# Performance work log

Hardware: AMD Instinct MI355X
Metric: run time of the kernel (lower is better)

Reference implementation:

```python
import jax, jax.numpy as jnp
import numpy as np

N = 100000   # nodes
E = 800000   # edges
D = 128      # input dim
H = 128      # hidden dim
C = 2        # output classes
BN_EPS = 1e-5


def setup_inputs() -> dict:
    key = jax.random.key(0)
    ks = jax.random.split(key, 24)
    glorot = lambda k, shape: jax.random.normal(k, shape, dtype=jnp.float32) * np.sqrt(2.0 / (shape[0] + shape[1]))
    inp = {
        "x": jax.random.normal(ks[0], (N, D), dtype=jnp.float32),
        "edge_index": jax.random.randint(ks[1], (2, E), 0, N, dtype=jnp.int64),
        "W0": glorot(ks[2], (D, H)), "b0": jnp.zeros((H,), jnp.float32),
        "W1": glorot(ks[3], (H, H)), "b1": jnp.zeros((H,), jnp.float32),
        "W2": glorot(ks[4], (H, H)), "b2": jnp.zeros((H,), jnp.float32),
        "W3": glorot(ks[5], (H, C)), "b3": jnp.zeros((C,), jnp.float32),
        # BatchNorm (eval mode: running stats)
        "bn0_g": jax.random.normal(ks[6], (H,), dtype=jnp.float32) * 0.1 + 1.0,
        "bn0_b": jax.random.normal(ks[7], (H,), dtype=jnp.float32) * 0.1,
        "bn0_m": jax.random.normal(ks[8], (H,), dtype=jnp.float32) * 0.1,
        "bn0_v": jax.random.uniform(ks[9], (H,), dtype=jnp.float32) + 0.5,
        "bn1_g": jax.random.normal(ks[10], (H,), dtype=jnp.float32) * 0.1 + 1.0,
        "bn1_b": jax.random.normal(ks[11], (H,), dtype=jnp.float32) * 0.1,
        "bn1_m": jax.random.normal(ks[12], (H,), dtype=jnp.float32) * 0.1,
        "bn1_v": jax.random.uniform(ks[13], (H,), dtype=jnp.float32) + 0.5,
    }
    return inp


def _gcn_conv(h, W, b, src, dst, norm, self_norm):
    # GCNConv: D^-1/2 (A + I) D^-1/2 (h W) + b
    hw = h @ W                                             # [N, out]
    msg = hw[src] * norm[:, None]                          # [E, out] gather
    agg = jax.ops.segment_sum(msg, dst, num_segments=N)    # [N, out] scatter-add
    return agg + hw * self_norm[:, None] + b


def _bn_eval(h, g, b, m, v):
    return (h - m) * (g * jax.lax.rsqrt(v + BN_EPS)) + b


def reference(x, edge_index, W0, b0, W1, b1, W2, b2, W3, b3,
              bn0_g, bn0_b, bn0_m, bn0_v, bn1_g, bn1_b, bn1_m, bn1_v):
    src, dst = edge_index[0], edge_index[1]
    # symmetric normalization with self-loops
    deg = jax.ops.segment_sum(jnp.ones((E,), jnp.float32), dst, num_segments=N) + 1.0
    dis = jax.lax.rsqrt(deg)                 # deg >= 1, no inf
    norm = dis[src] * dis[dst]               # per-edge norm
    self_norm = dis * dis                    # self-loop norm

    # layer 0 (eval mode: dropout is identity)
    h = jax.nn.relu(_gcn_conv(x, W0, b0, src, dst, norm, self_norm))
    # layer 1: conv -> bn -> relu -> residual
    h_prev = h
    h = _gcn_conv(h, W1, b1, src, dst, norm, self_norm)
    h = jax.nn.relu(_bn_eval(h, bn0_g, bn0_b, bn0_m, bn0_v)) + h_prev
    # layer 2
    h_prev = h
    h = _gcn_conv(h, W2, b2, src, dst, norm, self_norm)
    h = jax.nn.relu(_bn_eval(h, bn1_g, bn1_b, bn1_m, bn1_v)) + h_prev
    # output layer
    h = _gcn_conv(h, W3, b3, src, dst, norm, self_norm)
    return jax.nn.log_softmax(h, axis=1)
```

## Files before the change

kernel.cpp:

```cpp
#include <hip/hip_runtime.h>
#include <hip/hip_bf16.h>
#include <type_traits>

#define NN 100000
#define NE 800000
#define HD 128
#define BN_EPS 1e-5f
#define NB_E_C 3125

typedef __bf16 bf16x8 __attribute__((ext_vector_type(8)));
typedef float  f32x4  __attribute__((ext_vector_type(4)));
typedef float  f32x2  __attribute__((ext_vector_type(2)));


__global__ __launch_bounds__(256) void count_prep_k(const int* __restrict__ ei, int* __restrict__ count,
                                                    int* __restrict__ rank,
                                                    const float* __restrict__ W0, const float* __restrict__ W1,
                                                    const float* __restrict__ W2, __bf16* __restrict__ WT,
                                                    const float* __restrict__ g0, const float* __restrict__ b0,
                                                    const float* __restrict__ m0, const float* __restrict__ v0,
                                                    const float* __restrict__ g1, const float* __restrict__ b1,
                                                    const float* __restrict__ m1, const float* __restrict__ v1,
                                                    float* __restrict__ A0, float* __restrict__ B0,
                                                    float* __restrict__ A1, float* __restrict__ B1) {
    int bid = blockIdx.x;
    int tid = threadIdx.x;
    if (bid < NB_E_C) {
        int e = bid * 256 + tid;
        if (e < NE) rank[e] = atomicAdd(&count[ei[NE + e]], 1);
    } else if (bid < NB_E_C + 3) {
        int w = bid - NB_E_C;
        const float* Ws[3] = {W0, W1, W2};
        const float* W = Ws[w];
        __bf16* T = WT + w * (HD * HD);
        #pragma unroll 4
        for (int it = 0; it < 64; ++it) {
            int idx = it * 256 + tid;
            int n = idx >> 7, k = idx & 127;
            T[idx] = (__bf16)W[k * HD + n];
        }
    } else {
        if (tid < 128) {
            float a = g0[tid] * rsqrtf(v0[tid] + BN_EPS);
            A0[tid] = a; B0[tid] = b0[tid] - m0[tid] * a;
        } else {
            int u = tid - 128;
            float a = g1[u] * rsqrtf(v1[u] + BN_EPS);
            A1[u] = a; B1[u] = b1[u] - m1[u] * a;
        }
    }
}

__global__ __launch_bounds__(256) void scan1_k(const int* __restrict__ count,
                                               int* __restrict__ rp, int* __restrict__ bsums,
                                               float* __restrict__ dis, float* __restrict__ selfn) {
    __shared__ int sm[256];
    int tid = threadIdx.x;
    int i = blockIdx.x * 256 + tid;
    int v = (i < NN) ? count[i] : 0;
    if (i < NN) {
        float deg = (float)v + 1.0f;
        float di = rsqrtf(deg);
        dis[i] = di;
        selfn[i] = di * di;
    }
    sm[tid] = v; __syncthreads();
    for (int off = 1; off < 256; off <<= 1) {
        int t = (tid >= off) ? sm[tid - off] : 0;
        __syncthreads();
        sm[tid] += t;
        __syncthreads();
    }
    if (i < NN) rp[i] = sm[tid] - v;
    if (tid == 255) bsums[blockIdx.x] = sm[tid];
}

__global__ __launch_bounds__(256) void scan23_k(int* __restrict__ rp, const int* __restrict__ bsums, int nb) {
    __shared__ int sm[256];
    int tid = threadIdx.x;
    int b = blockIdx.x;
    int partial = 0;
    for (int i = tid; i < b; i += 256) partial += bsums[i];
    sm[tid] = partial; __syncthreads();
    #pragma unroll
    for (int off = 128; off > 0; off >>= 1) {
        if (tid < off) sm[tid] += sm[tid + off];
        __syncthreads();
    }
    int prefix = sm[0];
    int i = b * 256 + tid;
    if (i < NN) rp[i] += prefix;
    if (i == 0) rp[NN] = NE;
}

__global__ __launch_bounds__(256) void scatter_k(const int* __restrict__ ei, const int* __restrict__ rp,
                                                 const int* __restrict__ rank, const float* __restrict__ dis,
                                                 uint2* __restrict__ edges) {
    int e = blockIdx.x * 256 + threadIdx.x;
    if (e >= NE) return;
    int s = ei[e], d = ei[NE + e];
    int pos = rp[d] + rank[e];
    edges[pos] = make_uint2((unsigned)s, __float_as_uint(dis[s] * dis[d]));
}


template <typename T>
__global__ __launch_bounds__(256, 5) void gemm128_k(const T* __restrict__ A, const __bf16* __restrict__ WTg,
                                                    __bf16* __restrict__ HW) {
    __shared__ __bf16 WL[128 * 128];
    const int tid = threadIdx.x;
    const int wid  = __builtin_amdgcn_readfirstlane(tid >> 6);
    const int lane = tid & 63;
    const int m = lane & 15, quad = lane >> 4;
    const int row_base = blockIdx.x * 64 + wid * 16;

    int r = row_base + m;
    if (r >= NN) r = NN - 1;
    bf16x8 afr[4];
    if constexpr (std::is_same<T, float>::value) {
        const float4* ap = (const float4*)(A + (size_t)r * HD);
        #pragma unroll
        for (int ks = 0; ks < 4; ++ks) {
            float4 x0 = ap[ks * 8 + quad * 2], x1 = ap[ks * 8 + quad * 2 + 1];
            bf16x8 a;
            a[0] = (__bf16)x0.x; a[1] = (__bf16)x0.y; a[2] = (__bf16)x0.z; a[3] = (__bf16)x0.w;
            a[4] = (__bf16)x1.x; a[5] = (__bf16)x1.y; a[6] = (__bf16)x1.z; a[7] = (__bf16)x1.w;
            afr[ks] = a;
        }
    } else {
        const bf16x8* ap = (const bf16x8*)(A + (size_t)r * HD);
        #pragma unroll
        for (int ks = 0; ks < 4; ++ks) afr[ks] = ap[ks * 4 + quad];
    }

    #pragma unroll
    for (int it = 0; it < 8; ++it) {
        int id = it * 256 + tid;
        int n = id >> 4, c = id & 15;
        int cs = c ^ (n >> 3);
        *(uint4*)&WL[n * 128 + cs * 8] = *(const uint4*)(WTg + n * HD + c * 8);
    }
    __syncthreads();

    f32x4 acc[8];
    #pragma unroll
    for (int ct = 0; ct < 8; ++ct) acc[ct] = (f32x4){0.f, 0.f, 0.f, 0.f};

    #pragma unroll
    for (int ks = 0; ks < 4; ++ks) {
        #pragma unroll
        for (int ct = 0; ct < 8; ++ct) {
            int n = m * 8 + ct;
            int cs = (ks * 4 + quad) ^ m;
            bf16x8 bfr = *(const bf16x8*)&WL[n * 128 + cs * 8];
            acc[ct] = __builtin_amdgcn_mfma_f32_16x16x32_bf16(afr[ks], bfr, acc[ct], 0, 0, 0);
        }
    }

    #pragma unroll
    for (int rr = 0; rr < 4; ++rr) {
        int row = row_base + quad * 4 + rr;
        if (row < NN) {
            bf16x8 v;
            #pragma unroll
            for (int ct = 0; ct < 8; ++ct) v[ct] = (__bf16)acc[ct][rr];
            *(bf16x8*)(HW + (size_t)row * HD + m * 8) = v;
        }
    }
}


__device__ __forceinline__ void acc8p(f32x2* acc, uint4 rv, float wt) {
    f32x2 w2 = {wt, wt};
    f32x2 x0 = {__uint_as_float(rv.x << 16), __uint_as_float(rv.x & 0xffff0000u)};
    f32x2 x1 = {__uint_as_float(rv.y << 16), __uint_as_float(rv.y & 0xffff0000u)};
    f32x2 x2 = {__uint_as_float(rv.z << 16), __uint_as_float(rv.z & 0xffff0000u)};
    f32x2 x3 = {__uint_as_float(rv.w << 16), __uint_as_float(rv.w & 0xffff0000u)};
    acc[0] = __builtin_elementwise_fma(x0, w2, acc[0]);
    acc[1] = __builtin_elementwise_fma(x1, w2, acc[1]);
    acc[2] = __builtin_elementwise_fma(x2, w2, acc[2]);
    acc[3] = __builtin_elementwise_fma(x3, w2, acc[3]);
}

__device__ __forceinline__ void unpack8(uint4 rv, float* f) {
    f[0] = __uint_as_float(rv.x << 16);         f[1] = __uint_as_float(rv.x & 0xffff0000u);
    f[2] = __uint_as_float(rv.y << 16);         f[3] = __uint_as_float(rv.y & 0xffff0000u);
    f[4] = __uint_as_float(rv.z << 16);         f[5] = __uint_as_float(rv.z & 0xffff0000u);
    f[6] = __uint_as_float(rv.w << 16);         f[7] = __uint_as_float(rv.w & 0xffff0000u);
}


__global__ __launch_bounds__(256) void agg0_k(const __bf16* __restrict__ hw, const int* __restrict__ rp,
                                              const uint2* __restrict__ edges,
                                              const float* __restrict__ selfn, const float* __restrict__ bias,
                                              __bf16* __restrict__ hb) {
    const int lane = threadIdx.x & 63;
    const int wid  = threadIdx.x >> 6;
    const int grp  = lane >> 4;
    const int m    = lane & 15;
    const int n = blockIdx.x * 16 + wid * 4 + grp;
    const int c0 = m * 8;
    const int L = NE - 1;

    const int e0 = rp[n], e1 = rp[n + 1];
    const float sn = selfn[n];
    uint4 rv_self = *(const uint4*)(hw + ((size_t)n << 7) + c0);

    f32x2 acc2[4];
    #pragma unroll
    for (int j = 0; j < 4; ++j) acc2[j] = (f32x2){0.f, 0.f};

    int e = e0;
    int cnt = e1 - e0;
    uint2 edA = edges[min(e,     L)];
    uint2 edB = edges[min(e + 1, L)];
    uint2 edC = edges[min(e + 2, L)];
    uint2 edD = edges[min(e + 3, L)];
    while (cnt >= 4) {
        uint4 r0 = *(const uint4*)(hw + ((size_t)edA.x << 7) + c0);
        uint4 r1 = *(const uint4*)(hw + ((size_t)edB.x << 7) + c0);
        uint4 r2 = *(const uint4*)(hw + ((size_t)edC.x << 7) + c0);
        uint4 r3 = *(const uint4*)(hw + ((size_t)edD.x << 7) + c0);
        uint2 nA = edges[min(e + 4, L)];
        uint2 nB = edges[min(e + 5, L)];
        uint2 nC = edges[min(e + 6, L)];
        uint2 nD = edges[min(e + 7, L)];
        acc8p(acc2, r0, __uint_as_float(edA.y));
        acc8p(acc2, r1, __uint_as_float(edB.y));
        acc8p(acc2, r2, __uint_as_float(edC.y));
        acc8p(acc2, r3, __uint_as_float(edD.y));
        edA = nA; edB = nB; edC = nC; edD = nD;
        e += 4; cnt -= 4;
    }
    if (cnt >= 2) {
        uint4 r0 = *(const uint4*)(hw + ((size_t)edA.x << 7) + c0);
        uint4 r1 = *(const uint4*)(hw + ((size_t)edB.x << 7) + c0);
        acc8p(acc2, r0, __uint_as_float(edA.y));
        acc8p(acc2, r1, __uint_as_float(edB.y));
        edA = edC;
        cnt -= 2;
    }
    if (cnt == 1) {
        uint4 rv = *(const uint4*)(hw + ((size_t)edA.x << 7) + c0);
        acc8p(acc2, rv, __uint_as_float(edA.y));
    }
    acc8p(acc2, rv_self, sn);

    float a8[8] = {acc2[0][0], acc2[0][1], acc2[1][0], acc2[1][1],
                   acc2[2][0], acc2[2][1], acc2[3][0], acc2[3][1]};
    float4 bs0 = *(const float4*)(bias + c0);
    float4 bs1 = *(const float4*)(bias + c0 + 4);
    float bf[8] = {bs0.x, bs0.y, bs0.z, bs0.w, bs1.x, bs1.y, bs1.z, bs1.w};
    bf16x8 v;
    #pragma unroll
    for (int j = 0; j < 8; ++j) v[j] = (__bf16)fmaxf(a8[j] + bf[j], 0.f);
    *(bf16x8*)(hb + ((size_t)n << 7) + c0) = v;
}


template <int MODE>
__global__ __launch_bounds__(512, 4) void aggw_k(const __bf16* __restrict__ hbI, const __bf16* __restrict__ WTg,
                                                 const int* __restrict__ rp, const uint2* __restrict__ edges,
                                                 const float* __restrict__ selfn, const float* __restrict__ bias,
                                                 const float* __restrict__ bnA, const float* __restrict__ bnB,
                                                 __bf16* __restrict__ hbO, const float* __restrict__ W3,
                                                 float2* __restrict__ hw3) {
    __shared__ __bf16 WLs[128 * 128];
    const int tid = threadIdx.x;
    const int wid  = tid >> 6;
    const int lane = tid & 63;
    const int grp  = lane >> 4;
    const int m    = lane & 15;
    const int n = blockIdx.x * 32 + wid * 4 + grp;
    const int c0 = m * 8;
    const int L = NE - 1;

    #pragma unroll
    for (int it = 0; it < 4; ++it) {
        int id = it * 512 + tid;
        int r = id >> 4, c = id & 15;
        int cs = c ^ (r >> 3);
        *(uint4*)&WLs[r * 128 + cs * 8] = *(const uint4*)(WTg + r * HD + c * 8);
    }
    __syncthreads();

    const int e0 = rp[n], e1 = rp[n + 1];
    const float sn = selfn[n];
    uint4 rv_self = *(const uint4*)(hbI + ((size_t)n << 7) + c0);

    f32x2 acc2[4];
    #pragma unroll
    for (int j = 0; j < 4; ++j) acc2[j] = (f32x2){0.f, 0.f};

    int e = e0;
    int cnt = e1 - e0;
    uint2 edA = edges[min(e,     L)];
    uint2 edB = edges[min(e + 1, L)];
    uint2 edC = edges[min(e + 2, L)];
    uint2 edD = edges[min(e + 3, L)];
    while (cnt >= 4) {
        uint4 r0 = *(const uint4*)(hbI + ((size_t)edA.x << 7) + c0);
        uint4 r1 = *(const uint4*)(hbI + ((size_t)edB.x << 7) + c0);
        uint4 r2 = *(const uint4*)(hbI + ((size_t)edC.x << 7) + c0);
        uint4 r3 = *(const uint4*)(hbI + ((size_t)edD.x << 7) + c0);
        uint2 nA = edges[min(e + 4, L)];
        uint2 nB = edges[min(e + 5, L)];
        uint2 nC = edges[min(e + 6, L)];
        uint2 nD = edges[min(e + 7, L)];
        acc8p(acc2, r0, __uint_as_float(edA.y));
        acc8p(acc2, r1, __uint_as_float(edB.y));
        acc8p(acc2, r2, __uint_as_float(edC.y));
        acc8p(acc2, r3, __uint_as_float(edD.y));
        edA = nA; edB = nB; edC = nC; edD = nD;
        e += 4; cnt -= 4;
    }
    if (cnt >= 2) {
        uint4 r0 = *(const uint4*)(hbI + ((size_t)edA.x << 7) + c0);
        uint4 r1 = *(const uint4*)(hbI + ((size_t)edB.x << 7) + c0);
        acc8p(acc2, r0, __uint_as_float(edA.y));
        acc8p(acc2, r1, __uint_as_float(edB.y));
        edA = edC;
        cnt -= 2;
    }
    if (cnt == 1) {
        uint4 rv = *(const uint4*)(hbI + ((size_t)edA.x << 7) + c0);
        acc8p(acc2, rv, __uint_as_float(edA.y));
    }
    acc8p(acc2, rv_self, sn);

    float a8[8] = {acc2[0][0], acc2[0][1], acc2[1][0], acc2[1][1],
                   acc2[2][0], acc2[2][1], acc2[3][0], acc2[3][1]};
    bf16x8 sv;
    #pragma unroll
    for (int j = 0; j < 8; ++j) sv[j] = (__bf16)a8[j];

    int4 svi = *(int4*)&sv;
    const int base = ((m >> 2) << 4) + grp;
    bf16x8 afr[4];
    #pragma unroll
    for (int ks = 0; ks < 4; ++ks) {
        int sl = base + ks * 4;
        int4 r;
        r.x = __shfl(svi.x, sl, 64);
        r.y = __shfl(svi.y, sl, 64);
        r.z = __shfl(svi.z, sl, 64);
        r.w = __shfl(svi.w, sl, 64);
        afr[ks] = *(bf16x8*)&r;
    }

    float4 bs0 = *(const float4*)(bias + c0);
    float4 bs1 = *(const float4*)(bias + c0 + 4);
    float4 a0v = *(const float4*)(bnA + c0), a1v = *(const float4*)(bnA + c0 + 4);
    float4 b0v = *(const float4*)(bnB + c0), b1v = *(const float4*)(bnB + c0 + 4);
    float bf[8] = {bs0.x, bs0.y, bs0.z, bs0.w, bs1.x, bs1.y, bs1.z, bs1.w};
    float Af[8] = {a0v.x, a0v.y, a0v.z, a0v.w, a1v.x, a1v.y, a1v.z, a1v.w};
    float Bf[8] = {b0v.x, b0v.y, b0v.z, b0v.w, b1v.x, b1v.y, b1v.z, b1v.w};
    float pr[8];
    unpack8(rv_self, pr);
    float w3f[16];
    if (MODE == 2) {
        const float4* wp3 = (const float4*)(W3 + m * 16);
        #pragma unroll
        for (int j = 0; j < 4; ++j) {
            float4 t = wp3[j];
            w3f[j * 4] = t.x; w3f[j * 4 + 1] = t.y; w3f[j * 4 + 2] = t.z; w3f[j * 4 + 3] = t.w;
        }
    }

    float h8[8];
    #pragma unroll
    for (int ct = 0; ct < 8; ++ct) {
        const int nW = m * 8 + ct;
        f32x4 acc = (f32x4){0.f, 0.f, 0.f, 0.f};
        #pragma unroll
        for (int ks = 0; ks < 4; ++ks) {
            int cs = (ks * 4 + grp) ^ m;
            bf16x8 bfr = *(const bf16x8*)&WLs[nW * 128 + cs * 8];
            acc = __builtin_amdgcn_mfma_f32_16x16x32_bf16(afr[ks], bfr, acc, 0, 0, 0);
        }
        float z = acc[0] + bf[ct];
        h8[ct] = fmaxf(fmaf(z, Af[ct], Bf[ct]), 0.f) + pr[ct];
    }

    if (MODE == 1) {
        bf16x8 v;
        #pragma unroll
        for (int j = 0; j < 8; ++j) v[j] = (__bf16)h8[j];
        *(bf16x8*)(hbO + ((size_t)n << 7) + c0) = v;
    } else {
        float p0 = 0.f, p1 = 0.f;
        #pragma unroll
        for (int j = 0; j < 8; ++j) {
            p0 = fmaf(h8[j], w3f[2 * j], p0);
            p1 = fmaf(h8[j], w3f[2 * j + 1], p1);
        }
        #pragma unroll
        for (int o = 1; o < 16; o <<= 1) {
            p0 += __shfl_xor(p0, o);
            p1 += __shfl_xor(p1, o);
        }
        if (m == 0) hw3[n] = make_float2(p0, p1);
    }
}


__global__ __launch_bounds__(256) void final_k(const float2* __restrict__ hw3, const int* __restrict__ rp,
                                               const uint2* __restrict__ edges,
                                               const float* __restrict__ selfn, const float* __restrict__ b3,
                                               float* __restrict__ out) {
    int n = blockIdx.x * 256 + threadIdx.x;
    if (n >= NN) return;
    const int L = NE - 1;
    float a0 = 0.f, a1 = 0.f;
    int e0 = rp[n], e1 = rp[n + 1];
    int cnt = e1 - e0;
    uint2 edA = edges[min(e0,     L)];
    uint2 edB = edges[min(e0 + 1, L)];
    int e = e0;
    while (cnt >= 2) {
        float2 v0 = hw3[edA.x];
        float2 v1 = hw3[edB.x];
        float w0 = __uint_as_float(edA.y), w1 = __uint_as_float(edB.y);
        edA = edges[min(e + 2, L)];
        edB = edges[min(e + 3, L)];
        a0 = fmaf(w0, v0.x, a0); a1 = fmaf(w0, v0.y, a1);
        a0 = fmaf(w1, v1.x, a0); a1 = fmaf(w1, v1.y, a1);
        e += 2; cnt -= 2;
    }
    if (cnt == 1) {
        float2 v = hw3[edA.x];
        float w = __uint_as_float(edA.y);
        a0 = fmaf(w, v.x, a0); a1 = fmaf(w, v.y, a1);
    }
    float sn = selfn[n];
    float2 hv = hw3[n];
    float z0 = a0 + sn * hv.x + b3[0];
    float z1 = a1 + sn * hv.y + b3[1];
    float mx = fmaxf(z0, z1);
    float l = mx + logf(expf(z0 - mx) + expf(z1 - mx));
    out[n * 2 + 0] = z0 - l;
    out[n * 2 + 1] = z1 - l;
}


extern "C" void kernel_launch(void* const* d_in, const int* in_sizes, int n_in,
                              void* d_out, int out_size, void* d_ws, size_t ws_size,
                              hipStream_t stream) {
    (void)in_sizes; (void)n_in; (void)out_size; (void)ws_size;

    const float* x   = (const float*)d_in[0];
    const int*   ei  = (const int*)d_in[1];
    const float* W0  = (const float*)d_in[2];
    const float* b0  = (const float*)d_in[3];
    const float* W1  = (const float*)d_in[4];
    const float* b1  = (const float*)d_in[5];
    const float* W2  = (const float*)d_in[6];
    const float* b2  = (const float*)d_in[7];
    const float* W3  = (const float*)d_in[8];
    const float* b3  = (const float*)d_in[9];
    const float* bn0g = (const float*)d_in[10];
    const float* bn0b = (const float*)d_in[11];
    const float* bn0m = (const float*)d_in[12];
    const float* bn0v = (const float*)d_in[13];
    const float* bn1g = (const float*)d_in[14];
    const float* bn1b = (const float*)d_in[15];
    const float* bn1m = (const float*)d_in[16];
    const float* bn1v = (const float*)d_in[17];
    float* out = (float*)d_out;

    char* p = (char*)d_ws;
    auto alloc = [&](size_t bytes) -> void* {
        void* r = (void*)p;
        p += (bytes + 255) & ~(size_t)255;
        return r;
    };
    __bf16*  hb    = (__bf16*)alloc((size_t)NN * HD * 2);
    __bf16*  hb2   = (__bf16*)alloc((size_t)NN * HD * 2);
    __bf16*  hw    = (__bf16*)alloc((size_t)NN * HD * 2);
    float2*  hw3   = (float2*)alloc((size_t)NN * 8);
    float*   dis   = (float*)alloc((size_t)NN * 4);
    float*   selfn = (float*)alloc((size_t)NN * 4);
    int*     count = (int*)alloc((size_t)NN * 4);
    int*     rp    = (int*)alloc((size_t)(NN + 1) * 4);
    uint2*   edges = (uint2*)alloc((size_t)NE * 8);
    int*     rank  = (int*)alloc((size_t)NE * 4);
    int*     bsums = (int*)alloc((size_t)512 * 4);
    float*   bnA0  = (float*)alloc(128 * 4);
    float*   bnB0  = (float*)alloc(128 * 4);
    float*   bnA1  = (float*)alloc(128 * 4);
    float*   bnB1  = (float*)alloc(128 * 4);
    __bf16*  WT    = (__bf16*)alloc((size_t)3 * HD * HD * 2);

    const int NB_N = (NN + 255) / 256;
    const int NB_G = (NN + 63) / 64;
    const int NB_A = (NN + 15) / 16;
    const int NB_W = (NN + 31) / 32;

    hipMemsetAsync(count, 0, (size_t)NN * 4, stream);

    count_prep_k<<<NB_E_C + 4, 256, 0, stream>>>(ei, count, rank,
                                                 W0, W1, W2, WT,
                                                 bn0g, bn0b, bn0m, bn0v, bn1g, bn1b, bn1m, bn1v,
                                                 bnA0, bnB0, bnA1, bnB1);
    scan1_k<<<NB_N, 256, 0, stream>>>(count, rp, bsums, dis, selfn);
    scan23_k<<<NB_N, 256, 0, stream>>>(rp, bsums, NB_N);
    scatter_k<<<NB_E_C, 256, 0, stream>>>(ei, rp, rank, dis, edges);

    gemm128_k<float><<<NB_G, 256, 0, stream>>>(x, WT, hw);
    agg0_k<<<NB_A, 256, 0, stream>>>(hw, rp, edges, selfn, b0, hb);
    aggw_k<1><<<NB_W, 512, 0, stream>>>(hb, WT + HD * HD, rp, edges, selfn, b1,
                                        bnA0, bnB0, hb2, nullptr, nullptr);
    aggw_k<2><<<NB_W, 512, 0, stream>>>(hb2, WT + 2 * HD * HD, rp, edges, selfn, b2,
                                        bnA1, bnB1, nullptr, W3, hw3);
    final_k<<<NB_N, 256, 0, stream>>>(hw3, rp, edges, selfn, b3, out);
}
```

Measured before the change: 312.5 us.

## Fuse layer-0 GEMM into edge-count prep kernel to overlap independent work

The x@W0 GEMM no longer runs as its own kernel. It is folded into the first prep kernel as extra blocks, so it runs alongside the edge degree counting and weight transposes, and the separate launch is removed. Each GEMM block now transposes W0 from fp32 straight into LDS using strided scalar loads, where it used to read a pre-transposed bf16 copy. This removes a launch and a serialization point. In exchange, every GEMM block does redundant uncoalesced W0 reads, and the whole fused kernel runs with the tighter launch bounds and the LDS allocation.

```diff
diff --git a/kernel.cpp b/kernel.cpp
--- a/kernel.cpp
+++ b/kernel.cpp
@@ -1,45 +1,45 @@
 #include <hip/hip_runtime.h>
 #include <hip/hip_bf16.h>
-#include <type_traits>
 
 #define NN 100000
 #define NE 800000
 #define HD 128
 #define BN_EPS 1e-5f
 #define NB_E_C 3125
+#define NB_G_C 1563
 
 typedef __bf16 bf16x8 __attribute__((ext_vector_type(8)));
 typedef float  f32x4  __attribute__((ext_vector_type(4)));
 typedef float  f32x2  __attribute__((ext_vector_type(2)));
 
 
-__global__ __launch_bounds__(256) void count_prep_k(const int* __restrict__ ei, int* __restrict__ count,
-                                                    int* __restrict__ rank,
-                                                    const float* __restrict__ W0, const float* __restrict__ W1,
-                                                    const float* __restrict__ W2, __bf16* __restrict__ WT,
-                                                    const float* __restrict__ g0, const float* __restrict__ b0,
-                                                    const float* __restrict__ m0, const float* __restrict__ v0,
-                                                    const float* __restrict__ g1, const float* __restrict__ b1,
-                                                    const float* __restrict__ m1, const float* __restrict__ v1,
-                                                    float* __restrict__ A0, float* __restrict__ B0,
-                                                    float* __restrict__ A1, float* __restrict__ B1) {
-    int bid = blockIdx.x;
-    int tid = threadIdx.x;
-    if (bid < NB_E_C) {
-        int e = bid * 256 + tid;
-        if (e < NE) rank[e] = atomicAdd(&count[ei[NE + e]], 1);
-    } else if (bid < NB_E_C + 3) {
-        int w = bid - NB_E_C;
-        const float* Ws[3] = {W0, W1, W2};
-        const float* W = Ws[w];
-        __bf16* T = WT + w * (HD * HD);
+__global__ __launch_bounds__(256, 4) void fused0_k(const int* __restrict__ ei, int* __restrict__ count,
+                                                   int* __restrict__ rank,
+                                                   const float* __restrict__ x, const float* __restrict__ W0,
+                                                   const float* __restrict__ W1, const float* __restrict__ W2,
+                                                   __bf16* __restrict__ WT, __bf16* __restrict__ hw,
+                                                   const float* __restrict__ g0, const float* __restrict__ b0,
+                                                   const float* __restrict__ m0, const float* __restrict__ v0,
+                                                   const float* __restrict__ g1, const float* __restrict__ b1,
+                                                   const float* __restrict__ m1, const float* __restrict__ v1,
+                                                   float* __restrict__ A0, float* __restrict__ B0,
+                                                   float* __restrict__ A1, float* __restrict__ B1) {
+    __shared__ __bf16 WL[128 * 128];
+    const int bid = blockIdx.x;
+    const int tid = threadIdx.x;
+
+    if (bid < 2) {
+        const float* W = (bid == 0) ? W1 : W2;
+        __bf16* T = WT + (bid + 1) * (HD * HD);
         #pragma unroll 4
         for (int it = 0; it < 64; ++it) {
             int idx = it * 256 + tid;
             int n = idx >> 7, k = idx & 127;
             T[idx] = (__bf16)W[k * HD + n];
         }
-    } else {
+        return;
+    }
+    if (bid == 2) {
         if (tid < 128) {
             float a = g0[tid] * rsqrtf(v0[tid] + BN_EPS);
             A0[tid] = a; B0[tid] = b0[tid] - m0[tid] * a;
@@ -47,6 +47,71 @@
             int u = tid - 128;
             float a = g1[u] * rsqrtf(v1[u] + BN_EPS);
             A1[u] = a; B1[u] = b1[u] - m1[u] * a;
+        }
+        return;
+    }
+    if (bid < 3 + NB_E_C) {
+        int e = (bid - 3) * 256 + tid;
+        if (e < NE) rank[e] = atomicAdd(&count[ei[NE + e]], 1);
+        return;
+    }
+
+    const int gb = bid - 3 - NB_E_C;
+    const int wid  = __builtin_amdgcn_readfirstlane(tid >> 6);
+    const int lane = tid & 63;
+    const int m = lane & 15, quad = lane >> 4;
+    const int row_base = gb * 64 + wid * 16;
+
+    int r = row_base + m;
+    if (r >= NN) r = NN - 1;
+    bf16x8 afr[4];
+    {
+        const float4* ap = (const float4*)(x + (size_t)r * HD);
+        #pragma unroll
+        for (int ks = 0; ks < 4; ++ks) {
+            float4 x0 = ap[ks * 8 + quad * 2], x1 = ap[ks * 8 + quad * 2 + 1];
+            bf16x8 a;
+            a[0] = (__bf16)x0.x; a[1] = (__bf16)x0.y; a[2] = (__bf16)x0.z; a[3] = (__bf16)x0.w;
+            a[4] = (__bf16)x1.x; a[5] = (__bf16)x1.y; a[6] = (__bf16)x1.z; a[7] = (__bf16)x1.w;
+            afr[ks] = a;
+        }
+    }
+
+    #pragma unroll
+    for (int it = 0; it < 8; ++it) {
+        int id = it * 256 + tid;
+        int n = id >> 4, c = id & 15;
+        int cs = c ^ (n >> 3);
+        bf16x8 v;
+        #pragma unroll
+        for (int j = 0; j < 8; ++j) v[j] = (__bf16)W0[(c * 8 + j) * HD + n];
+        *(bf16x8*)&WL[n * 128 + cs * 8] = v;
+    }
+    __syncthreads();
+
+    f32x4 acc[8];
+    #pragma unroll
+    for (int ct = 0; ct < 8; ++ct) acc[ct] = (f32x4){0.f, 0.f, 0.f, 0.f};
+
+    #pragma unroll
+    for (int ks = 0; ks < 4; ++ks) {
+        #pragma unroll
+        for (int ct = 0; ct < 8; ++ct) {
+            int n = m * 8 + ct;
+            int cs = (ks * 4 + quad) ^ m;
+            bf16x8 bfr = *(const bf16x8*)&WL[n * 128 + cs * 8];
+            acc[ct] = __builtin_amdgcn_mfma_f32_16x16x32_bf16(afr[ks], bfr, acc[ct], 0, 0, 0);
+        }
+    }
+
+    #pragma unroll
+    for (int rr = 0; rr < 4; ++rr) {
+        int row = row_base + quad * 4 + rr;
+        if (row < NN) {
+            bf16x8 v;
+            #pragma unroll
+            for (int ct = 0; ct < 8; ++ct) v[ct] = (__bf16)acc[ct][rr];
+            *(bf16x8*)(hw + (size_t)row * HD + m * 8) = v;
         }
     }
 }
@@ -101,72 +166,6 @@
     int s = ei[e], d = ei[NE + e];
     int pos = rp[d] + rank[e];
     edges[pos] = make_uint2((unsigned)s, __float_as_uint(dis[s] * dis[d]));
-}
-
-
-template <typename T>
-__global__ __launch_bounds__(256, 5) void gemm128_k(const T* __restrict__ A, const __bf16* __restrict__ WTg,
-                                                    __bf16* __restrict__ HW) {
-    __shared__ __bf16 WL[128 * 128];
-    const int tid = threadIdx.x;
-    const int wid  = __builtin_amdgcn_readfirstlane(tid >> 6);
-    const int lane = tid & 63;
-    const int m = lane & 15, quad = lane >> 4;
-    const int row_base = blockIdx.x * 64 + wid * 16;
-
-    int r = row_base + m;
-    if (r >= NN) r = NN - 1;
-    bf16x8 afr[4];
-    if constexpr (std::is_same<T, float>::value) {
-        const float4* ap = (const float4*)(A + (size_t)r * HD);
-        #pragma unroll
-        for (int ks = 0; ks < 4; ++ks) {
-            float4 x0 = ap[ks * 8 + quad * 2], x1 = ap[ks * 8 + quad * 2 + 1];
-            bf16x8 a;
-            a[0] = (__bf16)x0.x; a[1] = (__bf16)x0.y; a[2] = (__bf16)x0.z; a[3] = (__bf16)x0.w;
-            a[4] = (__bf16)x1.x; a[5] = (__bf16)x1.y; a[6] = (__bf16)x1.z; a[7] = (__bf16)x1.w;
-            afr[ks] = a;
-        }
-    } else {
-        const bf16x8* ap = (const bf16x8*)(A + (size_t)r * HD);
-        #pragma unroll
-        for (int ks = 0; ks < 4; ++ks) afr[ks] = ap[ks * 4 + quad];
-    }
-
-    #pragma unroll
-    for (int it = 0; it < 8; ++it) {
-        int id = it * 256 + tid;
-        int n = id >> 4, c = id & 15;
-        int cs = c ^ (n >> 3);
-        *(uint4*)&WL[n * 128 + cs * 8] = *(const uint4*)(WTg + n * HD + c * 8);
-    }
-    __syncthreads();
-
-    f32x4 acc[8];
-    #pragma unroll
-    for (int ct = 0; ct < 8; ++ct) acc[ct] = (f32x4){0.f, 0.f, 0.f, 0.f};
-
-    #pragma unroll
-    for (int ks = 0; ks < 4; ++ks) {
-        #pragma unroll
-        for (int ct = 0; ct < 8; ++ct) {
-            int n = m * 8 + ct;
-            int cs = (ks * 4 + quad) ^ m;
-            bf16x8 bfr = *(const bf16x8*)&WL[n * 128 + cs * 8];
-            acc[ct] = __builtin_amdgcn_mfma_f32_16x16x32_bf16(afr[ks], bfr, acc[ct], 0, 0, 0);
-        }
-    }
-
-    #pragma unroll
-    for (int rr = 0; rr < 4; ++rr) {
-        int row = row_base + quad * 4 + rr;
-        if (row < NN) {
-            bf16x8 v;
-            #pragma unroll
-            for (int ct = 0; ct < 8; ++ct) v[ct] = (__bf16)acc[ct][rr];
-            *(bf16x8*)(HW + (size_t)row * HD + m * 8) = v;
-        }
-    }
 }
 
 
@@ -492,21 +491,20 @@
     __bf16*  WT    = (__bf16*)alloc((size_t)3 * HD * HD * 2);
 
     const int NB_N = (NN + 255) / 256;
-    const int NB_G = (NN + 63) / 64;
     const int NB_A = (NN + 15) / 16;
     const int NB_W = (NN + 31) / 32;
 
     hipMemsetAsync(count, 0, (size_t)NN * 4, stream);
 
-    count_prep_k<<<NB_E_C + 4, 256, 0, stream>>>(ei, count, rank,
-                                                 W0, W1, W2, WT,
-                                                 bn0g, bn0b, bn0m, bn0v, bn1g, bn1b, bn1m, bn1v,
-                                                 bnA0, bnB0, bnA1, bnB1);
+    fused0_k<<<3 + NB_E_C + NB_G_C, 256, 0, stream>>>(ei, count, rank,
+                                                      x, W0, W1, W2, WT, hw,
+                                                      bn0g, bn0b, bn0m, bn0v,
+                                                      bn1g, bn1b, bn1m, bn1v,
+                                                      bnA0, bnB0, bnA1, bnB1);
     scan1_k<<<NB_N, 256, 0, stream>>>(count, rp, bsums, dis, selfn);
     scan23_k<<<NB_N, 256, 0, stream>>>(rp, bsums, NB_N);
     scatter_k<<<NB_E_C, 256, 0, stream>>>(ei, rp, rank, dis, edges);
 
-    gemm128_k<float><<<NB_G, 256, 0, stream>>>(x, WT, hw);
     agg0_k<<<NB_A, 256, 0, stream>>>(hw, rp, edges, selfn, b0, hb);
     aggw_k<1><<<NB_W, 512, 0, stream>>>(hb, WT + HD * HD, rp, edges, selfn, b1,
                                         bnA0, bnB0, hb2, nullptr, nullptr);
```

New measurement: 350.7 us. +12.2%, slower.
